# Performance work log

Hardware: AMD Instinct MI355X
Metric: run time of the kernel (lower is better)

Reference implementation:

```python
import jax, jax.numpy as jnp
import numpy as np
from jax import lax

PAD_ID = 0
V, E = 100000, 300          # word vocab / embedding dim
VC, EC, C = 100, 50, 100    # char vocab / char emb dim / char conv channels
H, L = 256, 17              # lstm hidden / n_labels
B, S, LC = 32, 128, 50


def _conv1d(x, w, b):
    # x [B, Cin, T], w [Cout, Cin, K] -> valid conv
    y = lax.conv_general_dilated(x, w, window_strides=(1,), padding='VALID',
                                 dimension_numbers=('NCH', 'OIH', 'NCH'))
    return y + b[None, :, None]


def _lstm_dir(x_sbd, w_ih, w_hh, b, h0, c0):
    # x_sbd [S,B,D]; PyTorch gate order i,f,g,o
    def step(carry, x_t):
        h, c = carry
        g = x_t @ w_ih.T + h @ w_hh.T + b
        i, f, gg, o = jnp.split(g, 4, axis=-1)
        c = jax.nn.sigmoid(f) * c + jax.nn.sigmoid(i) * jnp.tanh(gg)
        h = jax.nn.sigmoid(o) * jnp.tanh(c)
        return (h, c), h
    _, hs = lax.scan(step, (h0, c0), x_sbd)
    return hs  # [S,B,H]


def _emissions(x, x_char, word_emb, char_emb,
               conv1_w, conv1_b, conv2_w, conv2_b, conv3_w, conv3_b,
               w_ih_f, w_hh_f, b_f, w_ih_b, w_hh_b, b_b, h0, c0, fc_w, fc_b):
    emb = word_emb[x]                                   # [B,S,E]
    ce = char_emb[x_char].transpose(0, 2, 1)            # [B,EC,LC]
    ce = jax.nn.relu(_conv1d(ce, conv1_w, conv1_b))
    ce = jax.nn.relu(_conv1d(ce, conv2_w, conv2_b))
    ce = jax.nn.relu(_conv1d(ce, conv3_w, conv3_b))
    pooled = ce.max(axis=2)                             # [B,C] (max over time)
    char_rep = jnp.broadcast_to(pooled[:, None, :], (emb.shape[0], emb.shape[1], pooled.shape[1]))
    xin = jnp.concatenate([emb, char_rep], axis=2)      # [B,S,E+C]
    xs = xin.transpose(1, 0, 2)                         # [S,B,D]
    hf = _lstm_dir(xs, w_ih_f, w_hh_f, b_f, h0[0], c0[0])
    hb = _lstm_dir(xs[::-1], w_ih_b, w_hh_b, b_b, h0[1], c0[1])[::-1]
    hcat = jnp.concatenate([hf, hb], axis=-1).transpose(1, 0, 2)  # [B,S,2H]
    em = hcat @ fc_w.T + fc_b                           # [B,S,L]
    return jax.nn.softmax(em, axis=1)                   # faithful: softmax over seq dim


def _viterbi(emissions, mask, start_t, trans, end_t):
    # emissions [B,S,L], mask [B,S]
    em = emissions.transpose(1, 0, 2)                   # [S,B,L]
    m = mask.T                                          # [S,B]
    score0 = start_t[None, :] + em[0]                   # [B,L]

    def fwd(score, inp):
        e_t, m_t = inp
        cand = score[:, :, None] + trans[None] + e_t[:, None, :]  # [B,L,L]
        nscore = cand.max(axis=1)
        idx = cand.argmax(axis=1).astype(jnp.int32)
        score = jnp.where(m_t[:, None] > 0, nscore, score)
        return score, idx

    score, hist = lax.scan(fwd, score0, (em[1:], m[1:]))  # hist [S-1,B,L]
    score = score + end_t[None, :]
    last = jnp.argmax(score, axis=-1).astype(jnp.int32)   # [B]

    def back(cur, inp):
        h_t, m_t = inp
        prev = jnp.take_along_axis(h_t, cur[:, None], axis=1)[:, 0]
        cur = jnp.where(m_t > 0, prev, cur)
        return cur, cur

    _, tags_rev = lax.scan(back, last, (hist[::-1], m[1:][::-1]))
    tags = jnp.concatenate([tags_rev[::-1], last[None]], axis=0)  # [S,B]
    return tags.T                                                 # [B,S]


def setup_inputs() -> dict:
    key = jax.random.key(0)
    ks = jax.random.split(key, 24)
    f = lambda i, shape, s=0.1: (jax.random.normal(ks[i], shape, dtype=jnp.float32) * s)
    inp = {
        'x': jax.random.randint(ks[0], (B, S), 1, V),          # no PAD -> mask all ones
        'x_char': jax.random.randint(ks[1], (B, LC), 1, VC),
        'word_emb': f(2, (V, E), 1.0),
        'char_emb': f(3, (VC, EC), 1.0).at[PAD_ID].set(0.0),
        'conv1_w': f(4, (C, EC, 3)), 'conv1_b': f(5, (C,)),
        'conv2_w': f(6, (C, C, 4)), 'conv2_b': f(7, (C,)),
        'conv3_w': f(8, (C, C, 5)), 'conv3_b': f(9, (C,)),
        'w_ih_f': f(10, (4 * H, E + C)), 'w_hh_f': f(11, (4 * H, H)), 'b_f': f(12, (4 * H,)),
        'w_ih_b': f(13, (4 * H, E + C)), 'w_hh_b': f(14, (4 * H, H)), 'b_b': f(15, (4 * H,)),
        'h0': f(16, (2, B, H), 1.0), 'c0': f(17, (2, B, H), 1.0),
        'fc_w': f(18, (L, 2 * H)), 'fc_b': f(19, (L,)),
        'start_t': f(20, (L,)), 'trans': f(21, (L, L)), 'end_t': f(22, (L,)),
    }
    return inp


def reference(x, x_char, word_emb, char_emb, conv1_w, conv1_b, conv2_w, conv2_b,
              conv3_w, conv3_b, w_ih_f, w_hh_f, b_f, w_ih_b, w_hh_b, b_b,
              h0, c0, fc_w, fc_b, start_t, trans, end_t):
    mask = (x != PAD_ID).astype(jnp.float32)
    em = _emissions(x, x_char, word_emb, char_emb, conv1_w, conv1_b, conv2_w, conv2_b,
                    conv3_w, conv3_b, w_ih_f, w_hh_f, b_f, w_ih_b, w_hh_b, b_b,
                    h0, c0, fc_w, fc_b)
    return _viterbi(em, mask, start_t, trans, end_t)
```

## Files before the change

### kernel.cpp

```cpp
#include <hip/hip_runtime.h>
#include <cmath>

#define B_   32
#define S_   128
#define E_   300
#define C_   100
#define EC_  50
#define LC_  50
#define H_   256
#define G4_  1024
#define L_   17
#define DHID_ 400
#define SLAB_ 8192
#define SENT2_ 0x7E007E00u
#define KP_   208

#define MRB_HINIT 0
#define MNB_HINIT 256
#define MRB_PW    256
#define MNB_PW    64
#define MRB_PB1   320
#define MNB_PB1   128
#define NBLK_MISC 448

#define TRB_FC   0
#define TNB_FC   128
#define TRB_SMV  128
#define TNB_SMV  32
#define NBLK_TAIL 160
#define F_EM  6

typedef _Float16 half8 __attribute__((ext_vector_type(8)));
typedef float f32x4 __attribute__((ext_vector_type(4)));
typedef unsigned long long ull;
struct __align__(16) U2 { ull x, y; };

__device__ __forceinline__ unsigned pack_split(float v) {
  _Float16 hi = (fabsf(v) >= 6.104e-5f) ? (_Float16)v : (_Float16)0.0f;
  float hif = (float)hi;
  _Float16 lo = (_Float16)((v - hif) * 2048.0f);
  return (unsigned)__builtin_bit_cast(unsigned short, hi)
       | ((unsigned)__builtin_bit_cast(unsigned short, lo) << 16);
}

__device__ __forceinline__ void flag_signal(int* f) {
  __syncthreads();
  if (threadIdx.x == 0)
    __hip_atomic_fetch_add(f, 1, __ATOMIC_RELEASE, __HIP_MEMORY_SCOPE_AGENT);
}
__device__ __forceinline__ void flag_wait(const int* f, int target) {
  while (__hip_atomic_load(f, __ATOMIC_ACQUIRE, __HIP_MEMORY_SCOPE_AGENT) < target)
    __builtin_amdgcn_s_sleep(16);
}

__global__ void k_misc(const int* __restrict__ x, const float* __restrict__ word_emb,
                       const float* __restrict__ h0,
                       const float* __restrict__ w_ih_f, const float* __restrict__ w_ih_b,
                       unsigned* __restrict__ hfrag,
                       unsigned* __restrict__ apH, unsigned* __restrict__ apL,
                       unsigned* __restrict__ bpH, unsigned* __restrict__ bpL,
                       int* __restrict__ flags) {
  const int bid = blockIdx.x;
  const int tid = threadIdx.x;
  if (bid == 0 && tid < 128) flags[tid] = 0;

  if (bid < MRB_PW) {
    const int g0 = bid * 256 + tid;
    const int nth = MNB_HINIT * 256;
    const int htot = 2 * (S_ + 1) * SLAB_;
    for (int idx = g0; idx < htot; idx += nth) {
      int sd = idx / SLAB_;
      int within = idx % SLAB_;
      int t = sd % (S_ + 1), d = sd / (S_ + 1);
      if (t != 0) { hfrag[idx] = SENT2_; continue; }
      int m8 = within & 7;
      int lane = (within >> 3) & 63;
      int q = within >> 9;
      int Kt = q & 7, Nt = q >> 3;
      int m = m8 & 3, isLo = m8 >> 2;
      int k0 = Kt * 32 + (lane >> 4) * 8 + 2 * m;
      int b = Nt * 16 + (lane & 15);
      unsigned p0 = pack_split(h0[((size_t)d * B_ + b) * H_ + k0]);
      unsigned p1 = pack_split(h0[((size_t)d * B_ + b) * H_ + k0 + 1]);
      unsigned hiw = (p0 & 0xFFFFu) | (p1 << 16);
      unsigned low = (p0 >> 16) | (p1 & 0xFFFF0000u);
      hfrag[idx] = isLo ? low : hiw;
    }
    return;
  } else if (bid < MRB_PB1) {
    const int q = bid - MRB_PW;
    const int total = 2 * G4_ * KP_;
    for (int idx = q * 256 + tid; idx < total; idx += MNB_PW * 256) {
      int d = idx / (G4_ * KP_);
      int rem = idx % (G4_ * KP_);
      int j = rem / KP_, k2 = rem % KP_;
      const float* w2 = d ? w_ih_b : w_ih_f;
      float v0 = 0.f, v1 = 0.f;
      if (k2 < 200) { v0 = w2[(size_t)j * DHID_ + 2 * k2]; v1 = w2[(size_t)j * DHID_ + 2 * k2 + 1]; }
      unsigned p0 = pack_split(v0), p1 = pack_split(v1);
      apH[idx] = (p0 & 0xFFFFu) | (p1 << 16);
      apL[idx] = (p0 >> 16) | (p1 & 0xFFFF0000u);
    }
    return;
  } else {
    const int q = bid - MRB_PB1;
    if (tid < KP_) {
      int k2 = tid;
      for (int rr = 0; rr < 32; ++rr) {
        int r = q * 32 + rr;
        int t2 = r >> 5, b2 = r & 31;
        if (k2 < 150) {
          const float* e2 = word_emb + (size_t)x[b2 * S_ + t2] * E_;
          unsigned p0 = pack_split(e2[2 * k2]), p1 = pack_split(e2[2 * k2 + 1]);
          bpH[(size_t)r * KP_ + k2] = (p0 & 0xFFFFu) | (p1 << 16);
          bpL[(size_t)r * KP_ + k2] = (p0 >> 16) | (p1 & 0xFFFF0000u);
        } else if (k2 >= 200) {
          bpH[(size_t)r * KP_ + k2] = 0u;
          bpL[(size_t)r * KP_ + k2] = 0u;
        }
      }
    }
    return;
  }
}

__global__ void k_conv1(const int* __restrict__ x_char, const float* __restrict__ char_emb,
                        const float* __restrict__ w1, const float* __restrict__ b1,
                        float* __restrict__ out1) {
  int b = blockIdx.x;
  int ot = blockIdx.y;
  __shared__ float ce[EC_ * 52];
  __shared__ float wl[50 * 150];
  __shared__ int ids[LC_];
  int tid = threadIdx.x;
  if (tid < LC_) ids[tid] = x_char[b * LC_ + tid];
  __syncthreads();
  for (int idx = tid; idx < LC_ * EC_; idx += 256) {
    int t = idx / EC_, ec = idx % EC_;
    ce[ec * 52 + t] = char_emb[ids[t] * EC_ + ec];
  }
  int obase = ot * 50;
  for (int idx = tid; idx < 50 * 150; idx += 256)
    wl[idx] = w1[obase * 150 + idx];
  __syncthreads();
  for (int idx = tid; idx < 50 * 48; idx += 256) {
    int o = idx / 48, t = idx % 48;
    float acc = b1[obase + o];
    const float* wr = &wl[o * 150];
    for (int c = 0; c < EC_; ++c) {
      const float* ip = &ce[c * 52 + t];
      acc += wr[c * 3 + 0] * ip[0] + wr[c * 3 + 1] * ip[1] + wr[c * 3 + 2] * ip[2];
    }
    out1[((size_t)b * C_ + obase + o) * 48 + t] = fmaxf(acc, 0.0f);
  }
}

__global__ void k_conv2(const float* __restrict__ in, const float* __restrict__ w2,
                        const float* __restrict__ b2, float* __restrict__ out2) {
  int b = blockIdx.x, ot = blockIdx.y;
  __shared__ float il[C_ * 48];
  __shared__ float wl[25 * 400];
  int tid = threadIdx.x;
  for (int idx = tid; idx < C_ * 48; idx += 256) il[idx] = in[(size_t)b * C_ * 48 + idx];
  int obase = ot * 25;
  for (int idx = tid; idx < 25 * 400; idx += 256) wl[idx] = w2[obase * 400 + idx];
  __syncthreads();
  for (int idx = tid; idx < 25 * 45; idx += 256) {
    int o = idx / 45, t = idx % 45;
    float acc = b2[obase + o];
    const float* wr = &wl[o * 400];
    for (int c = 0; c < C_; ++c) {
      const float* ip = &il[c * 48 + t];
      acc += wr[c * 4 + 0] * ip[0] + wr[c * 4 + 1] * ip[1] +
             wr[c * 4 + 2] * ip[2] + wr[c * 4 + 3] * ip[3];
    }
    out2[((size_t)b * C_ + obase + o) * 45 + t] = fmaxf(acc, 0.0f);
  }
}

__global__ void k_conv3(const float* __restrict__ in, const float* __restrict__ w3,
                        const float* __restrict__ b3, float* __restrict__ pooled) {
  int b = blockIdx.x, ot = blockIdx.y;
  __shared__ float il[C_ * 45];
  __shared__ float wl[20 * 500];
  __shared__ float o3[20 * 44];
  int tid = threadIdx.x;
  for (int idx = tid; idx < C_ * 45; idx += 256) il[idx] = in[(size_t)b * C_ * 45 + idx];
  int obase = ot * 20;
  for (int idx = tid; idx < 20 * 500; idx += 256) wl[idx] = w3[obase * 500 + idx];
  __syncthreads();
  for (int idx = tid; idx < 20 * 41; idx += 256) {
    int o = idx / 41, t = idx % 41;
    float acc = b3[obase + o];
    const float* wr = &wl[o * 500];
    for (int c = 0; c < C_; ++c) {
      const float* ip = &il[c * 45 + t];
      acc += wr[c * 5 + 0] * ip[0] + wr[c * 5 + 1] * ip[1] + wr[c * 5 + 2] * ip[2] +
             wr[c * 5 + 3] * ip[3] + wr[c * 5 + 4] * ip[4];
    }
    o3[o * 44 + t] = fmaxf(acc, 0.0f);
  }
  __syncthreads();
  if (tid < 20) {
    float m = o3[tid * 44];
    for (int t = 1; t < 41; ++t) m = fmaxf(m, o3[tid * 44 + t]);
    pooled[b * C_ + obase + tid] = m;
  }
}

__global__ void k_pb2(const float* __restrict__ pooled,
                      unsigned* __restrict__ bpH, unsigned* __restrict__ bpL) {
  const int q = blockIdx.x;
  const int k2 = threadIdx.x;
  if (k2 < 150 || k2 >= 200) return;
  for (int rr = 0; rr < 32; ++rr) {
    int r = q * 32 + rr;
    int b2 = r & 31;
    float v0 = pooled[b2 * C_ + 2 * k2 - 300];
    float v1 = pooled[b2 * C_ + 2 * k2 - 299];
    unsigned p0 = pack_split(v0), p1 = pack_split(v1);
    bpH[(size_t)r * KP_ + k2] = (p0 & 0xFFFFu) | (p1 << 16);
    bpL[(size_t)r * KP_ + k2] = (p0 >> 16) | (p1 & 0xFFFF0000u);
  }
}

__global__ __launch_bounds__(256) void k_gemm(
    const unsigned* __restrict__ apH, const unsigned* __restrict__ apL,
    const unsigned* __restrict__ bpH, const unsigned* __restrict__ bpL,
    const float* __restrict__ b_f, const float* __restrict__ b_b,
    float* __restrict__ gi) {
  const int jt = blockIdx.x, rt = blockIdx.y, d = blockIdx.z;
  const int j0 = jt * 128, r0 = rt * 128;
  const int tid = threadIdx.x;
  const int w = tid >> 6, l = tid & 63;
  const int lx = l & 15, lq = l >> 4;

  __shared__ unsigned aH[2048], aL[2048], bH[2048], bL[2048];

  f32x4 acch[2][8], accl[2][8];
#pragma unroll
  for (int mt = 0; mt < 2; ++mt)
#pragma unroll
    for (int nt = 0; nt < 8; ++nt) {
      f32x4 z = {0.f, 0.f, 0.f, 0.f};
      acch[mt][nt] = z; accl[mt][nt] = z;
    }

  const int jr = tid >> 1, hh = tid & 1;
  const int q_st = jr >> 4, lane_lo = jr & 15;
  const unsigned* arH = apH + ((size_t)(d * G4_ + j0 + jr)) * KP_ + hh * 8;
  const unsigned* arL = apL + ((size_t)(d * G4_ + j0 + jr)) * KP_ + hh * 8;
  const unsigned* brH = bpH + ((size_t)(r0 + jr)) * KP_ + hh * 8;
  const unsigned* brL = bpL + ((size_t)(r0 + jr)) * KP_ + hh * 8;
  const int w0 = (q_st * 64 + lane_lo + 32 * hh) * 4;
  const int w1 = (q_st * 64 + lane_lo + 32 * hh + 16) * 4;

  for (int Kt = 0; Kt < 13; ++Kt) {
    uint4 a0 = *(const uint4*)(arH + Kt * 16);
    uint4 a1 = *(const uint4*)(arH + Kt * 16 + 4);
    uint4 c0v = *(const uint4*)(arL + Kt * 16);
    uint4 c1v = *(const uint4*)(arL + Kt * 16 + 4);
    uint4 e0 = *(const uint4*)(brH + Kt * 16);
    uint4 e1 = *(const uint4*)(brH + Kt * 16 + 4);
    uint4 f0 = *(const uint4*)(brL + Kt * 16);
    uint4 f1 = *(const uint4*)(brL + Kt * 16 + 4);
    *(uint4*)&aH[w0] = a0; *(uint4*)&aH[w1] = a1;
    *(uint4*)&aL[w0] = c0v; *(uint4*)&aL[w1] = c1v;
    *(uint4*)&bH[w0] = e0; *(uint4*)&bH[w1] = e1;
    *(uint4*)&bL[w0] = f0; *(uint4*)&bL[w1] = f1;
    __syncthreads();

    union u4h { uint4 u; half8 h; };
    u4h AH0, AH1, AL0, AL1;
    AH0.u = *(const uint4*)&aH[((2 * w + 0) * 64 + l) * 4];
    AH1.u = *(const uint4*)&aH[((2 * w + 1) * 64 + l) * 4];
    AL0.u = *(const uint4*)&aL[((2 * w + 0) * 64 + l) * 4];
    AL1.u = *(const uint4*)&aL[((2 * w + 1) * 64 + l) * 4];
#pragma unroll
    for (int nt = 0; nt < 8; ++nt) {
      u4h BHn, BLn;
      BHn.u = *(const uint4*)&bH[(nt * 64 + l) * 4];
      BLn.u = *(const uint4*)&bL[(nt * 64 + l) * 4];
      acch[0][nt] = __builtin_amdgcn_mfma_f32_16x16x32_f16(AH0.h, BHn.h, acch[0][nt], 0, 0, 0);
      accl[0][nt] = __builtin_amdgcn_mfma_f32_16x16x32_f16(AH0.h, BLn.h, accl[0][nt], 0, 0, 0);
      accl[0][nt] = __builtin_amdgcn_mfma_f32_16x16x32_f16(AL0.h, BHn.h, accl[0][nt], 0, 0, 0);
      acch[1][nt] = __builtin_amdgcn_mfma_f32_16x16x32_f16(AH1.h, BHn.h, acch[1][nt], 0, 0, 0);
      accl[1][nt] = __builtin_amdgcn_mfma_f32_16x16x32_f16(AH1.h, BLn.h, accl[1][nt], 0, 0, 0);
      accl[1][nt] = __builtin_amdgcn_mfma_f32_16x16x32_f16(AL1.h, BHn.h, accl[1][nt], 0, 0, 0);
    }
    __syncthreads();
  }

  const float* bias = d ? b_b : b_f;
  const float inv2048 = 1.0f / 2048.0f;
#pragma unroll
  for (int mt = 0; mt < 2; ++mt) {
#pragma unroll
    for (int nt = 0; nt < 8; ++nt) {
      int rr = r0 + nt * 16 + lx;
      int tt = rr >> 5, bb = rr & 31;
      float* dst = gi + ((size_t)(d * S_ + tt) * G4_) * B_ + bb;
#pragma unroll
      for (int r4 = 0; r4 < 4; ++r4) {
        int j = j0 + (2 * w + mt) * 16 + lq * 4 + r4;
        dst[(size_t)j * B_] = acch[mt][nt][r4] + accl[mt][nt][r4] * inv2048 + bias[j];
      }
    }
  }
}

__global__ __launch_bounds__(256, 1) void k_lstm(
    const float* __restrict__ w_hh_f, const float* __restrict__ w_hh_b,
    const float* __restrict__ c0, const float* __restrict__ gi,
    float* __restrict__ hbuf, unsigned* __restrict__ hfrag) {
  const int iblk = blockIdx.x;
  const int d = blockIdx.y;
  const int Ktown = iblk >> 1;
  const int half = iblk & 1;
  const float* whh = d ? w_hh_b : w_hh_f;
  const int tid = threadIdx.x;
  const int w = tid >> 6;
  const int l = tid & 63;
  const int lx = l & 15, lq = l >> 4;
  const int u0 = iblk * 16;

  __shared__ ull slh[2048];
  __shared__ ull sll[2048];
  __shared__ float gl[4 * 16 * 33];
  __shared__ unsigned ps[2 * 576];

  half8 whi[8], wlo[8];
#pragma unroll
  for (int Kt = 0; Kt < 8; ++Kt) {
    int row = w * H_ + u0 + lx;
    int kk0 = Kt * 32 + lq * 8;
    const float* src = whh + (size_t)row * H_ + kk0;
    float4 f0 = *(const float4*)src;
    float4 f1 = *(const float4*)(src + 4);
    float wv[8] = {f0.x, f0.y, f0.z, f0.w, f1.x, f1.y, f1.z, f1.w};
    union { unsigned short s2[8]; half8 h; } HI, LO;
#pragma unroll
    for (int j = 0; j < 8; ++j) {
      float v = wv[j];
      _Float16 hi = (fabsf(v) >= 6.104e-5f) ? (_Float16)v : (_Float16)0.0f;
      float hif = (float)hi;
      _Float16 lo = (_Float16)((v - hif) * 2048.0f);
      HI.s2[j] = __builtin_bit_cast(unsigned short, hi);
      LO.s2[j] = __builtin_bit_cast(unsigned short, lo);
    }
    whi[Kt] = HI.h;
    wlo[Kt] = LO.h;
  }

  const int bc = tid & 31, cw = tid >> 5;
  float creg[2];
#pragma unroll
  for (int cu = 0; cu < 2; ++cu)
    creg[cu] = c0[((size_t)d * B_ + bc) * H_ + u0 + cu * 8 + cw];

  const int pNt = bc >> 4;
  const int pm = cw >> 1;
  const bool phi = (cw & 1) == 0;
  const int plane = bc & 15;
  const float inv2048 = 1.0f / 2048.0f;

  for (int t = 0; t < S_; ++t) {
    int torig = d ? (S_ - 1 - t) : t;

    f32x4 acch[2], accl[2];
    {
      const float* gbase = gi + ((size_t)(d * S_ + torig) * G4_) * B_;
#pragma unroll
      for (int Nt = 0; Nt < 2; ++Nt) {
        f32x4 v;
#pragma unroll
        for (int r = 0; r < 4; ++r) {
          int j = w * H_ + u0 + lq * 4 + r;
          v[r] = gbase[(size_t)j * B_ + Nt * 16 + lx];
        }
        acch[Nt] = v;
        f32x4 z = {0.f, 0.f, 0.f, 0.f};
        accl[Nt] = z;
      }
    }

    const ull* hp = (const ull*)(hfrag + (size_t)(d * (S_ + 1) + t) * SLAB_);
    ull pv[4][4];
#pragma unroll
    for (int c = 0; c < 4; ++c) {
      size_t base = ((size_t)(w * 4 + c) * 64 + l) * 4;
#pragma unroll
      for (int j = 0; j < 4; ++j)
        pv[c][j] = __hip_atomic_load(&hp[base + j], __ATOMIC_RELAXED,
                                     __HIP_MEMORY_SCOPE_AGENT);
    }
    for (;;) {
      bool pending = false;
#pragma unroll
      for (int c = 0; c < 4; ++c)
#pragma unroll
        for (int j = 0; j < 4; ++j)
          pending |= ((unsigned)pv[c][j] == SENT2_) |
                     ((unsigned)(pv[c][j] >> 32) == SENT2_);
      if (!pending) break;
#pragma unroll
      for (int c = 0; c < 4; ++c) {
        size_t base = ((size_t)(w * 4 + c) * 64 + l) * 4;
#pragma unroll
        for (int j = 0; j < 4; ++j)
          pv[c][j] = __hip_atomic_load(&hp[base + j], __ATOMIC_RELAXED,
                                       __HIP_MEMORY_SCOPE_AGENT);
      }
    }
#pragma unroll
    for (int c = 0; c < 4; ++c) {
      int idx = ((w * 4 + c) * 64 + l) * 2;
      U2 vh; vh.x = pv[c][0]; vh.y = pv[c][1];
      U2 vl; vl.x = pv[c][2]; vl.y = pv[c][3];
      *(U2*)&slh[idx] = vh;
      *(U2*)&sll[idx] = vl;
    }
    __syncthreads();

#pragma unroll
    for (int Kt = 0; Kt < 8; ++Kt) {
      half8 Bhi[2], Blo[2];
#pragma unroll
      for (int Nt = 0; Nt < 2; ++Nt) {
        int idx = ((Nt * 8 + Kt) * 64 + l) * 2;
        union { U2 u; half8 h; } UH, UL;
        UH.u = *(const U2*)&slh[idx];
        UL.u = *(const U2*)&sll[idx];
        Bhi[Nt] = UH.h;
        Blo[Nt] = UL.h;
      }
#pragma unroll
      for (int Nt = 0; Nt < 2; ++Nt) {
        acch[Nt] = __builtin_amdgcn_mfma_f32_16x16x32_f16(whi[Kt], Bhi[Nt], acch[Nt], 0, 0, 0);
        accl[Nt] = __builtin_amdgcn_mfma_f32_16x16x32_f16(whi[Kt], Blo[Nt], accl[Nt], 0, 0, 0);
        accl[Nt] = __builtin_amdgcn_mfma_f32_16x16x32_f16(wlo[Kt], Bhi[Nt], accl[Nt], 0, 0, 0);
      }
    }

#pragma unroll
    for (int Nt = 0; Nt < 2; ++Nt)
#pragma unroll
      for (int r = 0; r < 4; ++r) {
        int ul = lq * 4 + r;
        gl[(w * 16 + ul) * 33 + Nt * 16 + lx] = acch[Nt][r] + accl[Nt][r] * inv2048;
      }
    __syncthreads();

    float hreg[2];
#pragma unroll
    for (int cu = 0; cu < 2; ++cu) {
      int u = cu * 8 + cw;
      float g_i = gl[(0 * 16 + u) * 33 + bc];
      float g_f = gl[(1 * 16 + u) * 33 + bc];
      float g_g = gl[(2 * 16 + u) * 33 + bc];
      float g_o = gl[(3 * 16 + u) * 33 + bc];
      float si = 1.f / (1.f + __expf(-g_i));
      float sf = 1.f / (1.f + __expf(-g_f));
      float so = 1.f / (1.f + __expf(-g_o));
      float tg = 1.f - 2.f / (__expf(2.f * g_g) + 1.f);
      float cn = sf * creg[cu] + si * tg;
      float tc = 1.f - 2.f / (__expf(2.f * cn) + 1.f);
      float hn = so * tc;
      creg[cu] = cn;
      hreg[cu] = hn;
      unsigned me = pack_split(hn);
      unsigned pa = (unsigned)__shfl_xor((int)me, 32, 64);
      unsigned je = (cw & 1) ? pa : me;
      unsigned jo = (cw & 1) ? me : pa;
      unsigned hiw = (je & 0xFFFFu) | (jo << 16);
      unsigned low = (je >> 16) | (jo & 0xFFFF0000u);
      int lane2g = ((half * 2 + cu) << 4) | plane;
      int m8 = phi ? pm : (4 + pm);
      ps[pNt * 576 + lane2g * 9 + m8] = phi ? hiw : low;
    }
    __syncthreads();

    {
      ull* slab64 = (ull*)(hfrag + (size_t)(d * (S_ + 1) + t + 1) * SLAB_);
      int Nt = tid >> 7;
      int r = tid & 127;
      int lane2g = half * 32 + (r >> 2);
      int m2 = r & 3;
      unsigned a = ps[Nt * 576 + lane2g * 9 + 2 * m2];
      unsigned b2 = ps[Nt * 576 + lane2g * 9 + 2 * m2 + 1];
      ull v = (ull)a | ((ull)b2 << 32);
      __hip_atomic_store(&slab64[(size_t)(Nt * 8 + Ktown) * 256 + (size_t)half * 128 + r], v,
                         __ATOMIC_RELAXED, __HIP_MEMORY_SCOPE_AGENT);
      float* hb = hbuf + (size_t)(d * (S_ + 1) + t + 1) * (H_ * B_) + u0 * B_;
      hb[0 * 256 + tid] = hreg[0];
      hb[1 * 256 + tid] = hreg[1];
    }
  }
}

__global__ __launch_bounds__(256) void k_tail(
    const int* __restrict__ x, const float* __restrict__ hbuf,
    const float* __restrict__ fc_w, const float* __restrict__ fc_b,
    const float* __restrict__ start_t, const float* __restrict__ trans,
    const float* __restrict__ end_t,
    float* __restrict__ em, int* __restrict__ flags, int* __restrict__ out) {
  const int bid = blockIdx.x;
  union SMemTail {
    struct { float wT[512 * 18]; float psum[256 * 18]; } fc;
    struct { float e[S_ * L_]; float tr[L_ * L_]; float sc[2][L_];
             int hist[(S_ - 1) * L_]; int tags[S_]; } smv;
  };
  __shared__ SMemTail sm;

  if (bid < TRB_SMV) {
    const int s = bid;
    const int tid = threadIdx.x;
    float* wT = sm.fc.wT;
    float* psum = sm.fc.psum;
    for (int i = tid; i < L_ * 512; i += 256) {
      int l2 = i / 512, k = i % 512;
      wT[k * 18 + l2] = fc_w[i];
    }
    __syncthreads();
    const int b2 = tid & 31, kq = tid >> 5;
    const float* hf = hbuf + (size_t)(s + 1) * (H_ * B_);
    const float* hbk = hbuf + (size_t)(S_ + 1 + (S_ - s)) * (H_ * B_);
    float acc[L_];
#pragma unroll
    for (int l2 = 0; l2 < L_; ++l2) acc[l2] = 0.f;
    for (int i = 0; i < 64; ++i) {
      int k = kq * 64 + i;
      float hv = (k < 256) ? hf[k * 32 + b2] : hbk[(k - 256) * 32 + b2];
      const float* wr = &wT[k * 18];
#pragma unroll
      for (int l2 = 0; l2 < L_; ++l2) acc[l2] = fmaf(hv, wr[l2], acc[l2]);
    }
#pragma unroll
    for (int l2 = 0; l2 < L_; ++l2) psum[tid * 18 + l2] = acc[l2];
    __syncthreads();
    for (int idx = tid; idx < B_ * L_; idx += 256) {
      int bb2 = idx & 31, l2 = idx >> 5;
      float sum = fc_b[l2];
      for (int q2 = 0; q2 < 8; ++q2) sum += psum[(q2 * 32 + bb2) * 18 + l2];
      em[((size_t)bb2 * S_ + s) * L_ + l2] = sum;
    }
    flag_signal(&flags[F_EM]);
    return;
  } else {
    const int bb = bid - TRB_SMV;
    const int tid = threadIdx.x;
    float* e = sm.smv.e;
    float* tr = sm.smv.tr;
    auto sc = sm.smv.sc;
    int* hist = sm.smv.hist;
    int* tags = sm.smv.tags;

    if (tid == 0) flag_wait(&flags[F_EM], TNB_FC);
    __syncthreads();
    for (int i = tid; i < S_ * L_; i += 256) e[i] = em[(size_t)bb * S_ * L_ + i];
    for (int i = tid; i < L_ * L_; i += 256) tr[i] = trans[i];
    __syncthreads();
    if (tid < L_) {
      int l2 = tid;
      float m = -INFINITY;
      for (int s2 = 0; s2 < S_; ++s2) m = fmaxf(m, e[s2 * L_ + l2]);
      float sum2 = 0.f;
      for (int s2 = 0; s2 < S_; ++s2) {
        float ex = expf(e[s2 * L_ + l2] - m);
        e[s2 * L_ + l2] = ex;
        sum2 += ex;
      }
      for (int s2 = 0; s2 < S_; ++s2) e[s2 * L_ + l2] = e[s2 * L_ + l2] / sum2;
    }
    __syncthreads();
    if (tid < L_) sc[0][tid] = start_t[tid] + e[tid];
    __syncthreads();
    int cbuf = 0;
    for (int t2 = 1; t2 < S_; ++t2) {
      if (tid < L_) {
        int j2 = tid;
        float evv = e[t2 * L_ + j2];
        float best = -INFINITY;
        int arg = 0;
        for (int i = 0; i < L_; ++i) {
          float v = (sc[cbuf][i] + tr[i * L_ + j2]) + evv;
          if (v > best) { best = v; arg = i; }
        }
        int maskt = (x[bb * S_ + t2] != 0);
        sc[cbuf ^ 1][j2] = maskt ? best : sc[cbuf][j2];
        hist[(t2 - 1) * L_ + j2] = arg;
      }
      __syncthreads();
      cbuf ^= 1;
    }
    if (tid == 0) {
      float best = -INFINITY;
      int last = 0;
      for (int j2 = 0; j2 < L_; ++j2) {
        float v = sc[cbuf][j2] + end_t[j2];
        if (v > best) { best = v; last = j2; }
      }
      int cur = last;
      tags[S_ - 1] = cur;
      for (int p = S_ - 2; p >= 0; --p) {
        if (x[bb * S_ + p + 1] != 0) cur = hist[p * L_ + cur];
        tags[p] = cur;
      }
    }
    __syncthreads();
    for (int s2 = tid; s2 < S_; s2 += 256) out[bb * S_ + s2] = tags[s2];
    return;
  }
}

extern "C" void kernel_launch(void* const* d_in, const int* in_sizes, int n_in,
                              void* d_out, int out_size, void* d_ws, size_t ws_size,
                              hipStream_t stream) {
  const int* x        = (const int*)d_in[0];
  const int* x_char   = (const int*)d_in[1];
  const float* word_emb = (const float*)d_in[2];
  const float* char_emb = (const float*)d_in[3];
  const float* conv1_w = (const float*)d_in[4];
  const float* conv1_b = (const float*)d_in[5];
  const float* conv2_w = (const float*)d_in[6];
  const float* conv2_b = (const float*)d_in[7];
  const float* conv3_w = (const float*)d_in[8];
  const float* conv3_b = (const float*)d_in[9];
  const float* w_ih_f = (const float*)d_in[10];
  const float* w_hh_f = (const float*)d_in[11];
  const float* b_f    = (const float*)d_in[12];
  const float* w_ih_b = (const float*)d_in[13];
  const float* w_hh_b = (const float*)d_in[14];
  const float* b_b    = (const float*)d_in[15];
  const float* h0     = (const float*)d_in[16];
  const float* c0     = (const float*)d_in[17];
  const float* fc_w   = (const float*)d_in[18];
  const float* fc_b   = (const float*)d_in[19];
  const float* start_t = (const float*)d_in[20];
  const float* trans  = (const float*)d_in[21];
  const float* end_t  = (const float*)d_in[22];
  int* out = (int*)d_out;

  char* ws = (char*)d_ws;
  auto alloc = [&](size_t bytes) -> char* {
    char* p = ws;
    ws += (bytes + 1023) & ~(size_t)1023;
    return p;
  };
  float* pooled  = (float*)alloc(sizeof(float) * B_ * C_);
  float* gi      = (float*)alloc(sizeof(float) * 2 * S_ * G4_ * B_);
  float* hbuf    = (float*)alloc(sizeof(float) * 2 * (S_ + 1) * H_ * B_);
  unsigned* hfrag = (unsigned*)alloc(sizeof(unsigned) * 2 * (S_ + 1) * SLAB_);
  unsigned* apH  = (unsigned*)alloc(sizeof(unsigned) * 2 * G4_ * KP_);
  unsigned* apL  = (unsigned*)alloc(sizeof(unsigned) * 2 * G4_ * KP_);
  unsigned* bpH  = (unsigned*)alloc(sizeof(unsigned) * 4096 * KP_);
  unsigned* bpL  = (unsigned*)alloc(sizeof(unsigned) * 4096 * KP_);
  float* out1    = (float*)alloc(sizeof(float) * B_ * C_ * 48);
  float* out2    = (float*)alloc(sizeof(float) * B_ * C_ * 45);
  float* em      = (float*)alloc(sizeof(float) * B_ * S_ * L_);
  int* flags     = (int*)alloc(sizeof(int) * 128);

  k_misc<<<NBLK_MISC, 256, 0, stream>>>(x, word_emb, h0, w_ih_f, w_ih_b,
                                        hfrag, apH, apL, bpH, bpL, flags);
  k_conv1<<<dim3(32, 2), 256, 0, stream>>>(x_char, char_emb, conv1_w, conv1_b, out1);
  k_conv2<<<dim3(32, 4), 256, 0, stream>>>(out1, conv2_w, conv2_b, out2);
  k_conv3<<<dim3(32, 5), 256, 0, stream>>>(out2, conv3_w, conv3_b, pooled);
  k_pb2<<<128, 256, 0, stream>>>(pooled, bpH, bpL);
  k_gemm<<<dim3(8, 32, 2), 256, 0, stream>>>(apH, apL, bpH, bpL, b_f, b_b, gi);
  k_lstm<<<dim3(16, 2), 256, 0, stream>>>(w_hh_f, w_hh_b, c0, gi, hbuf, hfrag);
  k_tail<<<NBLK_TAIL, 256, 0, stream>>>(
      x, hbuf, fc_w, fc_b, start_t, trans, end_t, em, flags, out);
}
```

Measured before the change: 876.4 us.

## Fuse input-projection GEMM and LSTM recurrence into one persistent kernel with flags

Merges the separate gate-input GEMM and LSTM recurrence kernels into one launch. The first 32 blocks run the recurrence, while the remaining blocks pull GEMM tiles from an atomic work queue in time order (the backward direction in reverse) and raise per-row-tile flags. The LSTM waits on a flag only when it first needs a new tile of timesteps, so the recurrence can start before the whole GEMM finishes. Flags are padded to separate cache lines and the spin sleep is shortened. The risk is that spinning LSTM blocks share the GPU with GEMM blocks, and that progress depends on the GEMM blocks actually being scheduled alongside the LSTM blocks.

```diff
diff --git a/kernel.cpp b/kernel.cpp
--- a/kernel.cpp
+++ b/kernel.cpp
@@ -23,12 +23,21 @@
 #define MNB_PB1   128
 #define NBLK_MISC 448
 
+#define NB_LSTM   32
+#define NBLK_GL   544
+#define NTILE_G   512
+
 #define TRB_FC   0
 #define TNB_FC   128
 #define TRB_SMV  128
 #define TNB_SMV  32
 #define NBLK_TAIL 160
-#define F_EM  6
+
+#define F_EM   7
+#define FG(d, rt) (8 + (d) * 32 + (rt))
+#define Q_G    78
+#define FLG(i)    ((i) * 32)
+#define NFLAGS_   (80 * 32)
 
 typedef _Float16 half8 __attribute__((ext_vector_type(8)));
 typedef float f32x4 __attribute__((ext_vector_type(4)));
@@ -50,7 +59,7 @@
 }
 __device__ __forceinline__ void flag_wait(const int* f, int target) {
   while (__hip_atomic_load(f, __ATOMIC_ACQUIRE, __HIP_MEMORY_SCOPE_AGENT) < target)
-    __builtin_amdgcn_s_sleep(16);
+    __builtin_amdgcn_s_sleep(8);
 }
 
 __global__ void k_misc(const int* __restrict__ x, const float* __restrict__ word_emb,
@@ -62,7 +71,9 @@
                        int* __restrict__ flags) {
   const int bid = blockIdx.x;
   const int tid = threadIdx.x;
-  if (bid == 0 && tid < 128) flags[tid] = 0;
+  if (bid == 0) {
+    for (int i = tid; i < NFLAGS_; i += 256) flags[i] = 0;
+  }
 
   if (bid < MRB_PW) {
     const int g0 = bid * 256 + tid;
@@ -224,185 +235,111 @@
   }
 }
 
-__global__ __launch_bounds__(256) void k_gemm(
+union SMemGL {
+  char pad[84 * 1024];
+  struct { unsigned aH[2048], aL[2048], bH[2048], bL[2048]; } gemm;
+  struct { ull slh[2048], sll[2048]; float gl[4 * 16 * 33]; unsigned ps[2 * 576]; } lstm;
+};
+
+__global__ __launch_bounds__(256) void k_gl(
+    const float* __restrict__ w_hh_f, const float* __restrict__ w_hh_b,
+    const float* __restrict__ c0,
     const unsigned* __restrict__ apH, const unsigned* __restrict__ apL,
     const unsigned* __restrict__ bpH, const unsigned* __restrict__ bpL,
     const float* __restrict__ b_f, const float* __restrict__ b_b,
-    float* __restrict__ gi) {
-  const int jt = blockIdx.x, rt = blockIdx.y, d = blockIdx.z;
-  const int j0 = jt * 128, r0 = rt * 128;
+    float* __restrict__ gi, float* __restrict__ hbuf, unsigned* __restrict__ hfrag,
+    int* __restrict__ flags) {
+  const int bid = blockIdx.x;
   const int tid = threadIdx.x;
-  const int w = tid >> 6, l = tid & 63;
-  const int lx = l & 15, lq = l >> 4;
-
-  __shared__ unsigned aH[2048], aL[2048], bH[2048], bL[2048];
-
-  f32x4 acch[2][8], accl[2][8];
-#pragma unroll
-  for (int mt = 0; mt < 2; ++mt)
-#pragma unroll
-    for (int nt = 0; nt < 8; ++nt) {
-      f32x4 z = {0.f, 0.f, 0.f, 0.f};
-      acch[mt][nt] = z; accl[mt][nt] = z;
-    }
-
-  const int jr = tid >> 1, hh = tid & 1;
-  const int q_st = jr >> 4, lane_lo = jr & 15;
-  const unsigned* arH = apH + ((size_t)(d * G4_ + j0 + jr)) * KP_ + hh * 8;
-  const unsigned* arL = apL + ((size_t)(d * G4_ + j0 + jr)) * KP_ + hh * 8;
-  const unsigned* brH = bpH + ((size_t)(r0 + jr)) * KP_ + hh * 8;
-  const unsigned* brL = bpL + ((size_t)(r0 + jr)) * KP_ + hh * 8;
-  const int w0 = (q_st * 64 + lane_lo + 32 * hh) * 4;
-  const int w1 = (q_st * 64 + lane_lo + 32 * hh + 16) * 4;
-
-  for (int Kt = 0; Kt < 13; ++Kt) {
-    uint4 a0 = *(const uint4*)(arH + Kt * 16);
-    uint4 a1 = *(const uint4*)(arH + Kt * 16 + 4);
-    uint4 c0v = *(const uint4*)(arL + Kt * 16);
-    uint4 c1v = *(const uint4*)(arL + Kt * 16 + 4);
-    uint4 e0 = *(const uint4*)(brH + Kt * 16);
-    uint4 e1 = *(const uint4*)(brH + Kt * 16 + 4);
-    uint4 f0 = *(const uint4*)(brL + Kt * 16);
-    uint4 f1 = *(const uint4*)(brL + Kt * 16 + 4);
-    *(uint4*)&aH[w0] = a0; *(uint4*)&aH[w1] = a1;
-    *(uint4*)&aL[w0] = c0v; *(uint4*)&aL[w1] = c1v;
-    *(uint4*)&bH[w0] = e0; *(uint4*)&bH[w1] = e1;
-    *(uint4*)&bL[w0] = f0; *(uint4*)&bL[w1] = f1;
-    __syncthreads();
-
-    union u4h { uint4 u; half8 h; };
-    u4h AH0, AH1, AL0, AL1;
-    AH0.u = *(const uint4*)&aH[((2 * w + 0) * 64 + l) * 4];
-    AH1.u = *(const uint4*)&aH[((2 * w + 1) * 64 + l) * 4];
-    AL0.u = *(const uint4*)&aL[((2 * w + 0) * 64 + l) * 4];
-    AL1.u = *(const uint4*)&aL[((2 * w + 1) * 64 + l) * 4];
-#pragma unroll
-    for (int nt = 0; nt < 8; ++nt) {
-      u4h BHn, BLn;
-      BHn.u = *(const uint4*)&bH[(nt * 64 + l) * 4];
-      BLn.u = *(const uint4*)&bL[(nt * 64 + l) * 4];
-      acch[0][nt] = __builtin_amdgcn_mfma_f32_16x16x32_f16(AH0.h, BHn.h, acch[0][nt], 0, 0, 0);
-      accl[0][nt] = __builtin_amdgcn_mfma_f32_16x16x32_f16(AH0.h, BLn.h, accl[0][nt], 0, 0, 0);
-      accl[0][nt] = __builtin_amdgcn_mfma_f32_16x16x32_f16(AL0.h, BHn.h, accl[0][nt], 0, 0, 0);
-      acch[1][nt] = __builtin_amdgcn_mfma_f32_16x16x32_f16(AH1.h, BHn.h, acch[1][nt], 0, 0, 0);
-      accl[1][nt] = __builtin_amdgcn_mfma_f32_16x16x32_f16(AH1.h, BLn.h, accl[1][nt], 0, 0, 0);
-      accl[1][nt] = __builtin_amdgcn_mfma_f32_16x16x32_f16(AL1.h, BHn.h, accl[1][nt], 0, 0, 0);
-    }
-    __syncthreads();
-  }
-
-  const float* bias = d ? b_b : b_f;
-  const float inv2048 = 1.0f / 2048.0f;
-#pragma unroll
-  for (int mt = 0; mt < 2; ++mt) {
-#pragma unroll
-    for (int nt = 0; nt < 8; ++nt) {
-      int rr = r0 + nt * 16 + lx;
-      int tt = rr >> 5, bb = rr & 31;
-      float* dst = gi + ((size_t)(d * S_ + tt) * G4_) * B_ + bb;
-#pragma unroll
-      for (int r4 = 0; r4 < 4; ++r4) {
-        int j = j0 + (2 * w + mt) * 16 + lq * 4 + r4;
-        dst[(size_t)j * B_] = acch[mt][nt][r4] + accl[mt][nt][r4] * inv2048 + bias[j];
-      }
-    }
-  }
-}
-
-__global__ __launch_bounds__(256, 1) void k_lstm(
-    const float* __restrict__ w_hh_f, const float* __restrict__ w_hh_b,
-    const float* __restrict__ c0, const float* __restrict__ gi,
-    float* __restrict__ hbuf, unsigned* __restrict__ hfrag) {
-  const int iblk = blockIdx.x;
-  const int d = blockIdx.y;
-  const int Ktown = iblk >> 1;
-  const int half = iblk & 1;
-  const float* whh = d ? w_hh_b : w_hh_f;
-  const int tid = threadIdx.x;
-  const int w = tid >> 6;
-  const int l = tid & 63;
-  const int lx = l & 15, lq = l >> 4;
-  const int u0 = iblk * 16;
-
-  __shared__ ull slh[2048];
-  __shared__ ull sll[2048];
-  __shared__ float gl[4 * 16 * 33];
-  __shared__ unsigned ps[2 * 576];
-
-  half8 whi[8], wlo[8];
-#pragma unroll
-  for (int Kt = 0; Kt < 8; ++Kt) {
-    int row = w * H_ + u0 + lx;
-    int kk0 = Kt * 32 + lq * 8;
-    const float* src = whh + (size_t)row * H_ + kk0;
-    float4 f0 = *(const float4*)src;
-    float4 f1 = *(const float4*)(src + 4);
-    float wv[8] = {f0.x, f0.y, f0.z, f0.w, f1.x, f1.y, f1.z, f1.w};
-    union { unsigned short s2[8]; half8 h; } HI, LO;
-#pragma unroll
-    for (int j = 0; j < 8; ++j) {
-      float v = wv[j];
-      _Float16 hi = (fabsf(v) >= 6.104e-5f) ? (_Float16)v : (_Float16)0.0f;
-      float hif = (float)hi;
-      _Float16 lo = (_Float16)((v - hif) * 2048.0f);
-      HI.s2[j] = __builtin_bit_cast(unsigned short, hi);
-      LO.s2[j] = __builtin_bit_cast(unsigned short, lo);
-    }
-    whi[Kt] = HI.h;
-    wlo[Kt] = LO.h;
-  }
-
-  const int bc = tid & 31, cw = tid >> 5;
-  float creg[2];
-#pragma unroll
-  for (int cu = 0; cu < 2; ++cu)
-    creg[cu] = c0[((size_t)d * B_ + bc) * H_ + u0 + cu * 8 + cw];
-
-  const int pNt = bc >> 4;
-  const int pm = cw >> 1;
-  const bool phi = (cw & 1) == 0;
-  const int plane = bc & 15;
-  const float inv2048 = 1.0f / 2048.0f;
-
-  for (int t = 0; t < S_; ++t) {
-    int torig = d ? (S_ - 1 - t) : t;
-
-    f32x4 acch[2], accl[2];
-    {
-      const float* gbase = gi + ((size_t)(d * S_ + torig) * G4_) * B_;
-#pragma unroll
-      for (int Nt = 0; Nt < 2; ++Nt) {
-        f32x4 v;
-#pragma unroll
-        for (int r = 0; r < 4; ++r) {
-          int j = w * H_ + u0 + lq * 4 + r;
-          v[r] = gbase[(size_t)j * B_ + Nt * 16 + lx];
-        }
-        acch[Nt] = v;
-        f32x4 z = {0.f, 0.f, 0.f, 0.f};
-        accl[Nt] = z;
-      }
-    }
-
-    const ull* hp = (const ull*)(hfrag + (size_t)(d * (S_ + 1) + t) * SLAB_);
-    ull pv[4][4];
-#pragma unroll
-    for (int c = 0; c < 4; ++c) {
-      size_t base = ((size_t)(w * 4 + c) * 64 + l) * 4;
-#pragma unroll
-      for (int j = 0; j < 4; ++j)
-        pv[c][j] = __hip_atomic_load(&hp[base + j], __ATOMIC_RELAXED,
-                                     __HIP_MEMORY_SCOPE_AGENT);
-    }
-    for (;;) {
-      bool pending = false;
-#pragma unroll
-      for (int c = 0; c < 4; ++c)
-#pragma unroll
-        for (int j = 0; j < 4; ++j)
-          pending |= ((unsigned)pv[c][j] == SENT2_) |
-                     ((unsigned)(pv[c][j] >> 32) == SENT2_);
-      if (!pending) break;
+  __shared__ SMemGL sm;
+  __shared__ int curq;
+
+  if (bid < NB_LSTM) {
+    const int d = bid >> 4;
+    const int iblk = bid & 15;
+    const int Ktown = iblk >> 1;
+    const int half = iblk & 1;
+    const float* whh = d ? w_hh_b : w_hh_f;
+
+    const int w = tid >> 6;
+    const int l = tid & 63;
+    const int lx = l & 15, lq = l >> 4;
+    const int u0 = iblk * 16;
+
+    ull* slh = sm.lstm.slh;
+    ull* sll = sm.lstm.sll;
+    float* glb = sm.lstm.gl;
+    unsigned* ps = sm.lstm.ps;
+
+    half8 whi[8], wlo[8];
+#pragma unroll
+    for (int Kt = 0; Kt < 8; ++Kt) {
+      int row = w * H_ + u0 + lx;
+      int kk0 = Kt * 32 + lq * 8;
+      const float* src = whh + (size_t)row * H_ + kk0;
+      float4 f0 = *(const float4*)src;
+      float4 f1 = *(const float4*)(src + 4);
+      float wv[8] = {f0.x, f0.y, f0.z, f0.w, f1.x, f1.y, f1.z, f1.w};
+      union { unsigned short s2[8]; half8 h; } HI, LO;
+#pragma unroll
+      for (int j = 0; j < 8; ++j) {
+        float v = wv[j];
+        _Float16 hi = (fabsf(v) >= 6.104e-5f) ? (_Float16)v : (_Float16)0.0f;
+        float hif = (float)hi;
+        _Float16 lo = (_Float16)((v - hif) * 2048.0f);
+        HI.s2[j] = __builtin_bit_cast(unsigned short, hi);
+        LO.s2[j] = __builtin_bit_cast(unsigned short, lo);
+      }
+      whi[Kt] = HI.h;
+      wlo[Kt] = LO.h;
+    }
+
+    const int bc = tid & 31, cw = tid >> 5;
+    float creg[2];
+#pragma unroll
+    for (int cu = 0; cu < 2; ++cu)
+      creg[cu] = c0[((size_t)d * B_ + bc) * H_ + u0 + cu * 8 + cw];
+
+    const int pNt = bc >> 4;
+    const int pm = cw >> 1;
+    const bool phi = (cw & 1) == 0;
+    const int plane = bc & 15;
+    const float inv2048 = 1.0f / 2048.0f;
+
+    int rt_have = -1;
+    for (int t = 0; t < S_; ++t) {
+      int torig = d ? (S_ - 1 - t) : t;
+
+      int rt = torig >> 2;
+      if (rt != rt_have) {
+        if (tid == 0) {
+          const int* gf = &flags[FLG(FG(d, rt))];
+          while (__hip_atomic_load(gf, __ATOMIC_ACQUIRE, __HIP_MEMORY_SCOPE_AGENT) < 8)
+            __builtin_amdgcn_s_sleep(2);
+        }
+        __syncthreads();
+        rt_have = rt;
+      }
+
+      f32x4 acch[2], accl[2];
+      {
+        const float* gbase = gi + ((size_t)(d * S_ + torig) * G4_) * B_;
+#pragma unroll
+        for (int Nt = 0; Nt < 2; ++Nt) {
+          f32x4 v;
+#pragma unroll
+          for (int r = 0; r < 4; ++r) {
+            int j = w * H_ + u0 + lq * 4 + r;
+            v[r] = gbase[(size_t)j * B_ + Nt * 16 + lx];
+          }
+          acch[Nt] = v;
+          f32x4 z = {0.f, 0.f, 0.f, 0.f};
+          accl[Nt] = z;
+        }
+      }
+
+      const ull* hp = (const ull*)(hfrag + (size_t)(d * (S_ + 1) + t) * SLAB_);
+      ull pv[4][4];
 #pragma unroll
       for (int c = 0; c < 4; ++c) {
         size_t base = ((size_t)(w * 4 + c) * 64 + l) * 4;
@@ -411,90 +348,208 @@
           pv[c][j] = __hip_atomic_load(&hp[base + j], __ATOMIC_RELAXED,
                                        __HIP_MEMORY_SCOPE_AGENT);
       }
-    }
-#pragma unroll
-    for (int c = 0; c < 4; ++c) {
-      int idx = ((w * 4 + c) * 64 + l) * 2;
-      U2 vh; vh.x = pv[c][0]; vh.y = pv[c][1];
-      U2 vl; vl.x = pv[c][2]; vl.y = pv[c][3];
-      *(U2*)&slh[idx] = vh;
-      *(U2*)&sll[idx] = vl;
-    }
-    __syncthreads();
-
-#pragma unroll
-    for (int Kt = 0; Kt < 8; ++Kt) {
-      half8 Bhi[2], Blo[2];
-#pragma unroll
-      for (int Nt = 0; Nt < 2; ++Nt) {
-        int idx = ((Nt * 8 + Kt) * 64 + l) * 2;
-        union { U2 u; half8 h; } UH, UL;
-        UH.u = *(const U2*)&slh[idx];
-        UL.u = *(const U2*)&sll[idx];
-        Bhi[Nt] = UH.h;
-        Blo[Nt] = UL.h;
-      }
-#pragma unroll
-      for (int Nt = 0; Nt < 2; ++Nt) {
-        acch[Nt] = __builtin_amdgcn_mfma_f32_16x16x32_f16(whi[Kt], Bhi[Nt], acch[Nt], 0, 0, 0);
-        accl[Nt] = __builtin_amdgcn_mfma_f32_16x16x32_f16(whi[Kt], Blo[Nt], accl[Nt], 0, 0, 0);
-        accl[Nt] = __builtin_amdgcn_mfma_f32_16x16x32_f16(wlo[Kt], Bhi[Nt], accl[Nt], 0, 0, 0);
-      }
-    }
-
-#pragma unroll
-    for (int Nt = 0; Nt < 2; ++Nt)
-#pragma unroll
-      for (int r = 0; r < 4; ++r) {
-        int ul = lq * 4 + r;
-        gl[(w * 16 + ul) * 33 + Nt * 16 + lx] = acch[Nt][r] + accl[Nt][r] * inv2048;
-      }
-    __syncthreads();
-
-    float hreg[2];
-#pragma unroll
-    for (int cu = 0; cu < 2; ++cu) {
-      int u = cu * 8 + cw;
-      float g_i = gl[(0 * 16 + u) * 33 + bc];
-      float g_f = gl[(1 * 16 + u) * 33 + bc];
-      float g_g = gl[(2 * 16 + u) * 33 + bc];
-      float g_o = gl[(3 * 16 + u) * 33 + bc];
-      float si = 1.f / (1.f + __expf(-g_i));
-      float sf = 1.f / (1.f + __expf(-g_f));
-      float so = 1.f / (1.f + __expf(-g_o));
-      float tg = 1.f - 2.f / (__expf(2.f * g_g) + 1.f);
-      float cn = sf * creg[cu] + si * tg;
-      float tc = 1.f - 2.f / (__expf(2.f * cn) + 1.f);
-      float hn = so * tc;
-      creg[cu] = cn;
-      hreg[cu] = hn;
-      unsigned me = pack_split(hn);
-      unsigned pa = (unsigned)__shfl_xor((int)me, 32, 64);
-      unsigned je = (cw & 1) ? pa : me;
-      unsigned jo = (cw & 1) ? me : pa;
-      unsigned hiw = (je & 0xFFFFu) | (jo << 16);
-      unsigned low = (je >> 16) | (jo & 0xFFFF0000u);
-      int lane2g = ((half * 2 + cu) << 4) | plane;
-      int m8 = phi ? pm : (4 + pm);
-      ps[pNt * 576 + lane2g * 9 + m8] = phi ? hiw : low;
-    }
-    __syncthreads();
-
-    {
-      ull* slab64 = (ull*)(hfrag + (size_t)(d * (S_ + 1) + t + 1) * SLAB_);
-      int Nt = tid >> 7;
-      int r = tid & 127;
-      int lane2g = half * 32 + (r >> 2);
-      int m2 = r & 3;
-      unsigned a = ps[Nt * 576 + lane2g * 9 + 2 * m2];
-      unsigned b2 = ps[Nt * 576 + lane2g * 9 + 2 * m2 + 1];
-      ull v = (ull)a | ((ull)b2 << 32);
-      __hip_atomic_store(&slab64[(size_t)(Nt * 8 + Ktown) * 256 + (size_t)half * 128 + r], v,
-                         __ATOMIC_RELAXED, __HIP_MEMORY_SCOPE_AGENT);
-      float* hb = hbuf + (size_t)(d * (S_ + 1) + t + 1) * (H_ * B_) + u0 * B_;
-      hb[0 * 256 + tid] = hreg[0];
-      hb[1 * 256 + tid] = hreg[1];
-    }
+      for (;;) {
+        bool pending = false;
+#pragma unroll
+        for (int c = 0; c < 4; ++c)
+#pragma unroll
+          for (int j = 0; j < 4; ++j)
+            pending |= ((unsigned)pv[c][j] == SENT2_) |
+                       ((unsigned)(pv[c][j] >> 32) == SENT2_);
+        if (!pending) break;
+#pragma unroll
+        for (int c = 0; c < 4; ++c) {
+          size_t base = ((size_t)(w * 4 + c) * 64 + l) * 4;
+#pragma unroll
+          for (int j = 0; j < 4; ++j)
+            pv[c][j] = __hip_atomic_load(&hp[base + j], __ATOMIC_RELAXED,
+                                         __HIP_MEMORY_SCOPE_AGENT);
+        }
+      }
+#pragma unroll
+      for (int c = 0; c < 4; ++c) {
+        int idx = ((w * 4 + c) * 64 + l) * 2;
+        U2 vh; vh.x = pv[c][0]; vh.y = pv[c][1];
+        U2 vl; vl.x = pv[c][2]; vl.y = pv[c][3];
+        *(U2*)&slh[idx] = vh;
+        *(U2*)&sll[idx] = vl;
+      }
+      __syncthreads();
+
+#pragma unroll
+      for (int Kt = 0; Kt < 8; ++Kt) {
+        half8 Bhi[2], Blo[2];
+#pragma unroll
+        for (int Nt = 0; Nt < 2; ++Nt) {
+          int idx = ((Nt * 8 + Kt) * 64 + l) * 2;
+          union { U2 u; half8 h; } UH, UL;
+          UH.u = *(const U2*)&slh[idx];
+          UL.u = *(const U2*)&sll[idx];
+          Bhi[Nt] = UH.h;
+          Blo[Nt] = UL.h;
+        }
+#pragma unroll
+        for (int Nt = 0; Nt < 2; ++Nt) {
+          acch[Nt] = __builtin_amdgcn_mfma_f32_16x16x32_f16(whi[Kt], Bhi[Nt], acch[Nt], 0, 0, 0);
+          accl[Nt] = __builtin_amdgcn_mfma_f32_16x16x32_f16(whi[Kt], Blo[Nt], accl[Nt], 0, 0, 0);
+          accl[Nt] = __builtin_amdgcn_mfma_f32_16x16x32_f16(wlo[Kt], Bhi[Nt], accl[Nt], 0, 0, 0);
+        }
+      }
+
+#pragma unroll
+      for (int Nt = 0; Nt < 2; ++Nt)
+#pragma unroll
+        for (int r = 0; r < 4; ++r) {
+          int ul = lq * 4 + r;
+          glb[(w * 16 + ul) * 33 + Nt * 16 + lx] = acch[Nt][r] + accl[Nt][r] * inv2048;
+        }
+      __syncthreads();
+
+      float hreg[2];
+#pragma unroll
+      for (int cu = 0; cu < 2; ++cu) {
+        int u = cu * 8 + cw;
+        float g_i = glb[(0 * 16 + u) * 33 + bc];
+        float g_f = glb[(1 * 16 + u) * 33 + bc];
+        float g_g = glb[(2 * 16 + u) * 33 + bc];
+        float g_o = glb[(3 * 16 + u) * 33 + bc];
+        float si = 1.f / (1.f + __expf(-g_i));
+        float sf = 1.f / (1.f + __expf(-g_f));
+        float so = 1.f / (1.f + __expf(-g_o));
+        float tg = 1.f - 2.f / (__expf(2.f * g_g) + 1.f);
+        float cn = sf * creg[cu] + si * tg;
+        float tc = 1.f - 2.f / (__expf(2.f * cn) + 1.f);
+        float hn = so * tc;
+        creg[cu] = cn;
+        hreg[cu] = hn;
+        unsigned me = pack_split(hn);
+        unsigned pa = (unsigned)__shfl_xor((int)me, 32, 64);
+        unsigned je = (cw & 1) ? pa : me;
+        unsigned jo = (cw & 1) ? me : pa;
+        unsigned hiw = (je & 0xFFFFu) | (jo << 16);
+        unsigned low = (je >> 16) | (jo & 0xFFFF0000u);
+        int lane2g = ((half * 2 + cu) << 4) | plane;
+        int m8 = phi ? pm : (4 + pm);
+        ps[pNt * 576 + lane2g * 9 + m8] = phi ? hiw : low;
+      }
+      __syncthreads();
+
+      {
+        ull* slab64 = (ull*)(hfrag + (size_t)(d * (S_ + 1) + t + 1) * SLAB_);
+        int Nt = tid >> 7;
+        int r = tid & 127;
+        int lane2g = half * 32 + (r >> 2);
+        int m2 = r & 3;
+        unsigned a = ps[Nt * 576 + lane2g * 9 + 2 * m2];
+        unsigned b2 = ps[Nt * 576 + lane2g * 9 + 2 * m2 + 1];
+        ull v = (ull)a | ((ull)b2 << 32);
+        __hip_atomic_store(&slab64[(size_t)(Nt * 8 + Ktown) * 256 + (size_t)half * 128 + r], v,
+                           __ATOMIC_RELAXED, __HIP_MEMORY_SCOPE_AGENT);
+        float* hb = hbuf + (size_t)(d * (S_ + 1) + t + 1) * (H_ * B_) + u0 * B_;
+        hb[0 * 256 + tid] = hreg[0];
+        hb[1 * 256 + tid] = hreg[1];
+      }
+    }
+    return;
+  }
+
+  {
+    const int w = tid >> 6, l = tid & 63;
+    const int lx = l & 15, lq = l >> 4;
+    const int jr = tid >> 1, hh = tid & 1;
+    const int q_st = jr >> 4, lane_lo = jr & 15;
+    const int w0 = (q_st * 64 + lane_lo + 32 * hh) * 4;
+    const int w1 = (q_st * 64 + lane_lo + 32 * hh + 16) * 4;
+    unsigned* aH = sm.gemm.aH;
+    unsigned* aL = sm.gemm.aL;
+    unsigned* bH = sm.gemm.bH;
+    unsigned* bL = sm.gemm.bL;
+
+    for (;;) {
+      __syncthreads();
+      if (tid == 0)
+        curq = __hip_atomic_fetch_add(&flags[FLG(Q_G)], 1, __ATOMIC_RELAXED,
+                                      __HIP_MEMORY_SCOPE_AGENT);
+      __syncthreads();
+      const int g = curq;
+      if (g >= NTILE_G) break;
+      const int d = g & 1;
+      const int jt = (g >> 1) & 7;
+      const int rtb = g >> 4;
+      const int rt = d ? (31 - rtb) : rtb;
+      const int j0 = jt * 128, r0 = rt * 128;
+
+      f32x4 acch[2][8], accl[2][8];
+#pragma unroll
+      for (int mt = 0; mt < 2; ++mt)
+#pragma unroll
+        for (int nt = 0; nt < 8; ++nt) {
+          f32x4 z = {0.f, 0.f, 0.f, 0.f};
+          acch[mt][nt] = z; accl[mt][nt] = z;
+        }
+
+      const unsigned* arH = apH + ((size_t)(d * G4_ + j0 + jr)) * KP_ + hh * 8;
+      const unsigned* arL = apL + ((size_t)(d * G4_ + j0 + jr)) * KP_ + hh * 8;
+      const unsigned* brH = bpH + ((size_t)(r0 + jr)) * KP_ + hh * 8;
+      const unsigned* brL = bpL + ((size_t)(r0 + jr)) * KP_ + hh * 8;
+
+      for (int Kt = 0; Kt < 13; ++Kt) {
+        uint4 a0 = *(const uint4*)(arH + Kt * 16);
+        uint4 a1 = *(const uint4*)(arH + Kt * 16 + 4);
+        uint4 c0v = *(const uint4*)(arL + Kt * 16);
+        uint4 c1v = *(const uint4*)(arL + Kt * 16 + 4);
+        uint4 e0 = *(const uint4*)(brH + Kt * 16);
+        uint4 e1 = *(const uint4*)(brH + Kt * 16 + 4);
+        uint4 f0 = *(const uint4*)(brL + Kt * 16);
+        uint4 f1 = *(const uint4*)(brL + Kt * 16 + 4);
+        *(uint4*)&aH[w0] = a0; *(uint4*)&aH[w1] = a1;
+        *(uint4*)&aL[w0] = c0v; *(uint4*)&aL[w1] = c1v;
+        *(uint4*)&bH[w0] = e0; *(uint4*)&bH[w1] = e1;
+        *(uint4*)&bL[w0] = f0; *(uint4*)&bL[w1] = f1;
+        __syncthreads();
+
+        union u4h { uint4 u; half8 h; };
+        u4h AH0, AH1, AL0, AL1;
+        AH0.u = *(const uint4*)&aH[((2 * w + 0) * 64 + l) * 4];
+        AH1.u = *(const uint4*)&aH[((2 * w + 1) * 64 + l) * 4];
+        AL0.u = *(const uint4*)&aL[((2 * w + 0) * 64 + l) * 4];
+        AL1.u = *(const uint4*)&aL[((2 * w + 1) * 64 + l) * 4];
+#pragma unroll
+        for (int nt = 0; nt < 8; ++nt) {
+          u4h BHn, BLn;
+          BHn.u = *(const uint4*)&bH[(nt * 64 + l) * 4];
+          BLn.u = *(const uint4*)&bL[(nt * 64 + l) * 4];
+          acch[0][nt] = __builtin_amdgcn_mfma_f32_16x16x32_f16(AH0.h, BHn.h, acch[0][nt], 0, 0, 0);
+          accl[0][nt] = __builtin_amdgcn_mfma_f32_16x16x32_f16(AH0.h, BLn.h, accl[0][nt], 0, 0, 0);
+          accl[0][nt] = __builtin_amdgcn_mfma_f32_16x16x32_f16(AL0.h, BHn.h, accl[0][nt], 0, 0, 0);
+          acch[1][nt] = __builtin_amdgcn_mfma_f32_16x16x32_f16(AH1.h, BHn.h, acch[1][nt], 0, 0, 0);
+          accl[1][nt] = __builtin_amdgcn_mfma_f32_16x16x32_f16(AH1.h, BLn.h, accl[1][nt], 0, 0, 0);
+          accl[1][nt] = __builtin_amdgcn_mfma_f32_16x16x32_f16(AL1.h, BHn.h, accl[1][nt], 0, 0, 0);
+        }
+        __syncthreads();
+      }
+
+      const float* bias = d ? b_b : b_f;
+      const float inv2048 = 1.0f / 2048.0f;
+#pragma unroll
+      for (int mt = 0; mt < 2; ++mt) {
+#pragma unroll
+        for (int nt = 0; nt < 8; ++nt) {
+          int rr = r0 + nt * 16 + lx;
+          int tt = rr >> 5, bb2 = rr & 31;
+          unsigned* dst = (unsigned*)gi + ((size_t)(d * S_ + tt) * G4_) * B_ + bb2;
+#pragma unroll
+          for (int r4 = 0; r4 < 4; ++r4) {
+            int j = j0 + (2 * w + mt) * 16 + lq * 4 + r4;
+            float vv = acch[mt][nt][r4] + accl[mt][nt][r4] * inv2048 + bias[j];
+            __hip_atomic_store(&dst[(size_t)j * B_], __builtin_bit_cast(unsigned, vv),
+                               __ATOMIC_RELAXED, __HIP_MEMORY_SCOPE_AGENT);
+          }
+        }
+      }
+      flag_signal(&flags[FLG(FG(d, rt))]);
+    }
+    return;
   }
 }
 
@@ -544,7 +599,7 @@
       for (int q2 = 0; q2 < 8; ++q2) sum += psum[(q2 * 32 + bb2) * 18 + l2];
       em[((size_t)bb2 * S_ + s) * L_ + l2] = sum;
     }
-    flag_signal(&flags[F_EM]);
+    flag_signal(&flags[FLG(F_EM)]);
     return;
   } else {
     const int bb = bid - TRB_SMV;
@@ -555,7 +610,7 @@
     int* hist = sm.smv.hist;
     int* tags = sm.smv.tags;
 
-    if (tid == 0) flag_wait(&flags[F_EM], TNB_FC);
+    if (tid == 0) flag_wait(&flags[FLG(F_EM)], TNB_FC);
     __syncthreads();
     for (int i = tid; i < S_ * L_; i += 256) e[i] = em[(size_t)bb * S_ * L_ + i];
     for (int i = tid; i < L_ * L_; i += 256) tr[i] = trans[i];
@@ -658,7 +713,7 @@
   float* out1    = (float*)alloc(sizeof(float) * B_ * C_ * 48);
   float* out2    = (float*)alloc(sizeof(float) * B_ * C_ * 45);
   float* em      = (float*)alloc(sizeof(float) * B_ * S_ * L_);
-  int* flags     = (int*)alloc(sizeof(int) * 128);
+  int* flags     = (int*)alloc(sizeof(int) * NFLAGS_);
 
   k_misc<<<NBLK_MISC, 256, 0, stream>>>(x, word_emb, h0, w_ih_f, w_ih_b,
                                         hfrag, apH, apL, bpH, bpL, flags);
@@ -666,8 +721,8 @@
   k_conv2<<<dim3(32, 4), 256, 0, stream>>>(out1, conv2_w, conv2_b, out2);
   k_conv3<<<dim3(32, 5), 256, 0, stream>>>(out2, conv3_w, conv3_b, pooled);
   k_pb2<<<128, 256, 0, stream>>>(pooled, bpH, bpL);
-  k_gemm<<<dim3(8, 32, 2), 256, 0, stream>>>(apH, apL, bpH, bpL, b_f, b_b, gi);
-  k_lstm<<<dim3(16, 2), 256, 0, stream>>>(w_hh_f, w_hh_b, c0, gi, hbuf, hfrag);
+  k_gl<<<NBLK_GL, 256, 0, stream>>>(w_hh_f, w_hh_b, c0, apH, apL, bpH, bpL,
+                                    b_f, b_b, gi, hbuf, hfrag, flags);
   k_tail<<<NBLK_TAIL, 256, 0, stream>>>(
       x, hbuf, fc_w, fc_b, start_t, trans, end_t, em, flags, out);
 }
```

Result: no change. 866.8 us (-1.1%).
